# Performance work log

Hardware: AMD Instinct MI355X
Metric: run time of the kernel (lower is better)

Reference implementation:

```python
import jax, jax.numpy as jnp
import numpy as np
from jax import lax


def setup_inputs() -> dict:
    key = jax.random.key(0)
    kw, ku, kk, kv = jax.random.split(key, 4)
    B, H, W, C = 8, 16, 16, 256
    # w is a positive per-channel decay (offset keeps exp(sum relu(...)) numerically sane);
    # k, u scaled down like trained RWKV params to avoid exp overflow in the reference.
    w = jax.random.uniform(kw, (C,), dtype=jnp.float32) + 0.3
    u = jax.random.normal(ku, (C,), dtype=jnp.float32) * 0.1
    k = jax.random.normal(kk, (B, H, W, C), dtype=jnp.float32) * 0.1
    v = jax.random.normal(kv, (B, H, W, C), dtype=jnp.float32)
    return {"B": B, "H": H, "W": W, "C": C, "w": w, "u": u, "k": k, "v": v}


def _wkv2d(B, H, W, C, w, u, k, v):
    # kernel covers the whole feature map
    K = 2 * (max(H, W) - 1) + 1
    pad = K // 2
    c = K // 2
    # Manhattan-distance decay weights, (C, K, K), with bonus u at the center.
    coords = jnp.arange(K)
    dist = (jnp.abs(coords[None, :] - c) + jnp.abs(coords[:, None] - c)).astype(w.dtype)
    wmat = -dist[None, :, :] * w[:, None, None]
    wmat = wmat.at[:, c, c].add(u)
    wflat = wmat.reshape(C, K * K).T  # (K*K, C)

    k_chw = jnp.transpose(k, (0, 3, 1, 2))  # (B,C,H,W)
    k_pad = jnp.pad(k_chw, ((0, 0), (0, 0), (pad, pad), (pad, pad)))  # zero pad == F.unfold padding

    idx = jnp.arange(K * K, dtype=jnp.int32)
    dys, dxs = idx // K, idx % K

    # Fused windowed relu-sum: never materialize the (B,C,K^2,HW) unfold tensor.
    def body(acc, xs):
        dy, dx, wc = xs
        win = lax.dynamic_slice(k_pad, (0, 0, dy, dx), (B, C, H, W))
        return acc + jax.nn.relu(win + wc[None, :, None, None]), None

    acc0 = jnp.zeros((B, C, H, W), dtype=k.dtype)
    k_adj, _ = lax.scan(body, acc0, (dys, dxs, wflat))

    v_chw = jnp.transpose(v, (0, 3, 1, 2))
    out = jnp.exp(k_adj) * v_chw  # (B,C,H,W)
    return jnp.transpose(out, (0, 2, 3, 1))  # back to (B,H,W,C)


def reference(B, H, W, C, w, u, k, v):
    return _wkv2d(B, H, W, C, w, u, k, v)
```

## Files before the change

kernel.cpp:

```cpp
#include <hip/hip_runtime.h>
#include <math.h>


constexpr int Bq = 8, Hq = 16, Wq = 16, Cq = 256;
constexpr int HW = Hq * Wq;
constexpr int CG = 16;
constexpr int YT = 2;
constexpr int ROWP = HW + 4;

__global__ __launch_bounds__(256, 4)
void wkv2d_kernel(const float* __restrict__ w,
                  const float* __restrict__ u,
                  const float* __restrict__ k,
                  const float* __restrict__ v,
                  float* __restrict__ out) {
    __shared__ float klds[CG][ROWP];

    const int bid = blockIdx.x;
    const int y0  = (bid & 7) * YT;
    const int c0  = ((bid >> 3) & 15) * CG;
    const int b   = bid >> 7;

    const int tid = threadIdx.x;
    const int cl  = tid & 15;
    const int x   = tid >> 4;

    {
        #pragma unroll
        for (int i = 0; i < 4; ++i) {
            const int f = tid + 256 * i;
            const int p = f >> 2;
            const int q = f & 3;
            const float4 kv = ((const float4*)(k + ((size_t)(b * HW + p)) * Cq + c0))[q];
            klds[4 * q + 0][p] = kv.x;
            klds[4 * q + 1][p] = kv.y;
            klds[4 * q + 2][p] = kv.z;
            klds[4 * q + 3][p] = kv.w;
        }
    }
    __syncthreads();

    const int   c  = c0 + cl;
    const float wc = w[c];
    const float fx = (float)x;
    const float fy0 = (float)y0;

    float wxv[16];
    #pragma unroll
    for (int rx = 0; rx < 16; ++rx)
        wxv[rx] = fabsf((float)rx - fx) * wc;

    float acc0 = 0.f, acc1 = 0.f;
    const float* krow = &klds[cl][0];

    #pragma unroll
    for (int ry = 0; ry < 16; ++ry) {
        const float fy  = (float)ry;
        const float wy0 = fabsf(fy - fy0) * wc;
        const float wy1 = fabsf(fy - fy0 - 1.0f) * wc;

        const float4* rr = (const float4*)(krow + ry * 16);
        #pragma unroll
        for (int j = 0; j < 4; ++j) {
            const float4 r = rr[j];
            const float rv[4] = {r.x, r.y, r.z, r.w};
            #pragma unroll
            for (int t = 0; t < 4; ++t) {
                const float t0 = rv[t] - wxv[4 * j + t];
                acc0 += fmaxf(t0 - wy0, 0.f);
                acc1 += fmaxf(t0 - wy1, 0.f);
            }
        }
    }

    const float uc  = u[c];
    const float ks0 = krow[(y0 + 0) * 16 + x];
    const float ks1 = krow[(y0 + 1) * 16 + x];
    const float a0 = acc0 + fmaxf(ks0 + uc, 0.f) - fmaxf(ks0, 0.f);
    const float a1 = acc1 + fmaxf(ks1 + uc, 0.f) - fmaxf(ks1, 0.f);

    const size_t idx0 = ((size_t)((b * 16 + y0) * 16 + x)) * Cq + c;
    const size_t idx1 = idx0 + (size_t)Wq * Cq;
    out[idx0] = __expf(a0) * v[idx0];
    out[idx1] = __expf(a1) * v[idx1];
}

extern "C" void kernel_launch(void* const* d_in, const int* in_sizes, int n_in,
                              void* d_out, int out_size, void* d_ws, size_t ws_size,
                              hipStream_t stream) {
    const float* w = (const float*)d_in[4];
    const float* u = (const float*)d_in[5];
    const float* k = (const float*)d_in[6];
    const float* v = (const float*)d_in[7];
    float* out = (float*)d_out;

    const int grid = Bq * (Cq / CG) * (Hq / YT);
    wkv2d_kernel<<<grid, 256, 0, stream>>>(w, u, k, v, out);
}
```

Measured before the change: 81.09 us.

## Compute four output rows per thread and rewrite relu-sum as max minus offset

Each block now covers four output rows (YT=4) instead of two, so the k tile staged in LDS is reused across more outputs and the grid shrinks to half as many blocks. The inner relu accumulation uses max(t0, wy) summed per row and then subtracts 16*wy, which removes one subtraction per element. Launch bounds drop to 2 blocks per SM to leave room for the extra accumulators. The trade-offs are fewer blocks available to spread across the GPU, and the accumulation order change may alter floating-point rounding slightly.

```diff
diff --git a/kernel.cpp b/kernel.cpp
--- a/kernel.cpp
+++ b/kernel.cpp
@@ -5,10 +5,10 @@
 constexpr int Bq = 8, Hq = 16, Wq = 16, Cq = 256;
 constexpr int HW = Hq * Wq;
 constexpr int CG = 16;
-constexpr int YT = 2;
+constexpr int YT = 4;
 constexpr int ROWP = HW + 4;
 
-__global__ __launch_bounds__(256, 4)
+__global__ __launch_bounds__(256, 2)
 void wkv2d_kernel(const float* __restrict__ w,
                   const float* __restrict__ u,
                   const float* __restrict__ k,
@@ -17,47 +17,48 @@
     __shared__ float klds[CG][ROWP];
 
     const int bid = blockIdx.x;
-    const int y0  = (bid & 7) * YT;
-    const int c0  = ((bid >> 3) & 15) * CG;
-    const int b   = bid >> 7;
+    const int y0  = (bid & 3) * YT;
+    const int c0  = ((bid >> 2) & 15) * CG;
+    const int b   = bid >> 6;
 
     const int tid = threadIdx.x;
     const int cl  = tid & 15;
     const int x   = tid >> 4;
 
-    {
-        #pragma unroll
-        for (int i = 0; i < 4; ++i) {
-            const int f = tid + 256 * i;
-            const int p = f >> 2;
-            const int q = f & 3;
-            const float4 kv = ((const float4*)(k + ((size_t)(b * HW + p)) * Cq + c0))[q];
-            klds[4 * q + 0][p] = kv.x;
-            klds[4 * q + 1][p] = kv.y;
-            klds[4 * q + 2][p] = kv.z;
-            klds[4 * q + 3][p] = kv.w;
-        }
+    #pragma unroll
+    for (int i = 0; i < 4; ++i) {
+        const int f = tid + 256 * i;
+        const int p = f >> 2;
+        const int q = f & 3;
+        const float4 kv = ((const float4*)(k + ((size_t)(b * HW + p)) * Cq + c0))[q];
+        klds[4 * q + 0][p] = kv.x;
+        klds[4 * q + 1][p] = kv.y;
+        klds[4 * q + 2][p] = kv.z;
+        klds[4 * q + 3][p] = kv.w;
     }
     __syncthreads();
 
     const int   c  = c0 + cl;
     const float wc = w[c];
     const float fx = (float)x;
-    const float fy0 = (float)y0;
 
     float wxv[16];
     #pragma unroll
     for (int rx = 0; rx < 16; ++rx)
         wxv[rx] = fabsf((float)rx - fx) * wc;
 
-    float acc0 = 0.f, acc1 = 0.f;
+    float acc[4] = {0.f, 0.f, 0.f, 0.f};
     const float* krow = &klds[cl][0];
 
-    #pragma unroll
+    #pragma unroll 4
     for (int ry = 0; ry < 16; ++ry) {
-        const float fy  = (float)ry;
-        const float wy0 = fabsf(fy - fy0) * wc;
-        const float wy1 = fabsf(fy - fy0 - 1.0f) * wc;
+        const float fy = (float)ry;
+        float wy[4], rs[4];
+        #pragma unroll
+        for (int i = 0; i < 4; ++i) {
+            wy[i] = fabsf(fy - (float)(y0 + i)) * wc;
+            rs[i] = 0.f;
+        }
 
         const float4* rr = (const float4*)(krow + ry * 16);
         #pragma unroll
@@ -67,22 +68,24 @@
             #pragma unroll
             for (int t = 0; t < 4; ++t) {
                 const float t0 = rv[t] - wxv[4 * j + t];
-                acc0 += fmaxf(t0 - wy0, 0.f);
-                acc1 += fmaxf(t0 - wy1, 0.f);
+                #pragma unroll
+                for (int i = 0; i < 4; ++i)
+                    rs[i] += fmaxf(t0, wy[i]);
             }
         }
+        #pragma unroll
+        for (int i = 0; i < 4; ++i)
+            acc[i] += rs[i] - 16.0f * wy[i];
     }
 
-    const float uc  = u[c];
-    const float ks0 = krow[(y0 + 0) * 16 + x];
-    const float ks1 = krow[(y0 + 1) * 16 + x];
-    const float a0 = acc0 + fmaxf(ks0 + uc, 0.f) - fmaxf(ks0, 0.f);
-    const float a1 = acc1 + fmaxf(ks1 + uc, 0.f) - fmaxf(ks1, 0.f);
-
-    const size_t idx0 = ((size_t)((b * 16 + y0) * 16 + x)) * Cq + c;
-    const size_t idx1 = idx0 + (size_t)Wq * Cq;
-    out[idx0] = __expf(a0) * v[idx0];
-    out[idx1] = __expf(a1) * v[idx1];
+    const float uc = u[c];
+    #pragma unroll
+    for (int i = 0; i < 4; ++i) {
+        const float ks = krow[(y0 + i) * 16 + x];
+        const float a  = acc[i] + fmaxf(ks + uc, 0.f) - fmaxf(ks, 0.f);
+        const size_t idx = ((size_t)((b * 16 + y0 + i) * 16 + x)) * Cq + c;
+        out[idx] = __expf(a) * v[idx];
+    }
 }
 
 extern "C" void kernel_launch(void* const* d_in, const int* in_sizes, int n_in,
```

Result: no change. 81.87 us (+1.0%).
